# Kernel tuning notes

Hardware: AMD Instinct MI355X
Metric: run time of the kernel (lower is better)

Reference implementation:

```python
import jax, jax.numpy as jnp
import numpy as np

BIG = 1e10  # large finite value standing in for +inf in masked mins (grad-safe)


def setup_inputs() -> dict:
    key = jax.random.key(0)
    k1, k2, k3 = jax.random.split(key, 3)
    B, C, N = 16, 3, 4096
    x = jax.random.normal(k1, (B, C, N), dtype=jnp.float32)
    y = jax.random.normal(k2, (B, C, N), dtype=jnp.float32)
    mask = jax.random.randint(k3, (B, N), 0, 2, dtype=jnp.int32)
    return {"x": x, "y": y, "mask": mask}


def reference(x, y, mask):
    # x, y: (B, 3, N); mask: (B, N) with 1 = valid point
    xt = jnp.swapaxes(x, 1, 2)  # (B, N, 3)
    yt = jnp.swapaxes(y, 1, 2)  # (B, N, 3)
    xx = jnp.sum(xt * xt, axis=-1)  # (B, N)
    yy = jnp.sum(yt * yt, axis=-1)  # (B, N)
    # squared pairwise distances, P[b, n, m] = ||x_bn - y_bm||^2
    P = xx[:, :, None] + yy[:, None, :] - 2.0 * jnp.einsum("bnd,bmd->bnm", xt, yt)

    valid = mask.astype(bool)                 # (B, N)
    mf = mask.astype(P.dtype)                 # (B, N)
    cnt = jnp.sum(mf, axis=1)                 # (B,) number of valid points per batch

    # direction 1: for each y-point m, min over valid x-rows n; mean over valid m
    mins1 = jnp.min(jnp.where(valid[:, :, None], P, BIG), axis=1)  # (B, N)
    means1 = jnp.sum(mins1 * mf, axis=1) / cnt                      # (B,)

    # direction 2: for each x-point m, min over valid y-cols n; mean over valid m
    mins2 = jnp.min(jnp.where(valid[:, None, :], P, BIG), axis=2)  # (B, N)
    means2 = jnp.sum(mins2 * mf, axis=1) / cnt                      # (B,)

    return jnp.mean(means1) + jnp.mean(means2)
```

## Files before the change

### kernel.cpp

```cpp
#include <hip/hip_runtime.h>

typedef short bf16x8 __attribute__((ext_vector_type(8)));
typedef float f32x16 __attribute__((ext_vector_type(16)));

#define BIG_F 1e10f
constexpr int B = 16;
constexpr int N = 4096;
constexpr int COLS = 512;
constexpr int NCB = N / COLS;
constexpr int PASSES = 2;
constexpr int SUBROWS = 512;
constexpr int NSB = N / SUBROWS;

__device__ __forceinline__ void split(float v, unsigned& h, unsigned& l) {
    unsigned hb = __float_as_uint(v) & 0xFFFF0000u;
    h = hb >> 16;
    float r = v - __uint_as_float(hb);
    l = __float_as_uint(r) >> 16;
}

__device__ __forceinline__ float min3f(float a, float b, float c) {
    return fminf(fminf(a, b), c);
}

__device__ __forceinline__ float vmin16(f32x16 C) {
    float u0 = min3f(C[0], C[1], C[2]);
    float u1 = min3f(C[3], C[4], C[5]);
    float u2 = min3f(C[6], C[7], C[8]);
    float u3 = min3f(C[9], C[10], C[11]);
    float u4 = min3f(C[12], C[13], C[14]);
    return min3f(min3f(u0, u1, u2), fminf(u3, u4), C[15]);
}

__device__ __forceinline__ float4 min4(float4 a, float4 b) {
    return make_float4(fminf(a.x, b.x), fminf(a.y, b.y),
                       fminf(a.z, b.z), fminf(a.w, b.w));
}

#define DPP_MIN(v, ctrl)                                                      \
    v = fminf(v, __int_as_float(__builtin_amdgcn_update_dpp(                  \
            __float_as_int(v), __float_as_int(v), (ctrl), 0xF, 0xF, false)))

__global__ __launch_bounds__(256, 3) void chamfer_mfma(
    const float* __restrict__ x, const float* __restrict__ y,
    const int* __restrict__ mask,
    float* __restrict__ rowpart,
    float* __restrict__ colpart,
    float* __restrict__ out)
{
    const int blk = blockIdx.x;
    const int b   = blk >> 6;
    const int cb  = (blk >> 3) & 7;
    const int sub = blk & 7;
    const int t   = threadIdx.x;

    __shared__ __align__(16) unsigned short Bpack[2][COLS][8];
    __shared__ float colbuf[8][COLS];

    if (blk == 0 && t == 0) out[0] = 0.0f;

    const float* xb = x + (size_t)b * 3 * N;
    const float* yb = y + (size_t)b * 3 * N;
    const int*   mb = mask + b * N;

#pragma unroll
    for (int i = 0; i < 2; ++i) {
        int c = t + i * 256;
        int m = cb * COLS + c;
        float y0 = yb[m], y1 = yb[N + m], y2 = yb[2 * N + m];
        float madd = mb[m] ? 0.0f : BIG_F;
        float yy = fmaf(y2, y2, fmaf(y1, y1, y0 * y0)) + madd;
        unsigned h0, l0, h1, l1, h2, l2, qh, ql;
        split(y0, h0, l0);
        split(y1, h1, l1);
        split(y2, h2, l2);
        split(yy, qh, ql);
        unsigned u0 = h0 | (h1 << 16);
        unsigned u1 = h2 | (l0 << 16);
        unsigned u2 = l1 | (l2 << 16);
        uint4 w0 = { u0, u1, u2, u0 };
        uint4 w1 = { u1, u2, 0x3F803F80u, qh | (ql << 16) };
        *(uint4*)&Bpack[0][c][0] = w0;
        *(uint4*)&Bpack[1][c][0] = w1;
    }

    const int w    = t >> 6;
    const int L    = t & 63;
    const int half = L >> 5;
    const int lc   = L & 31;

    __syncthreads();

    const unsigned short* Bb = &Bpack[half][lc][0];
    float* cacc0 = &colbuf[w * 2 + half][lc];

    const f32x16 z16 = {0.f,0.f,0.f,0.f,0.f,0.f,0.f,0.f,
                        0.f,0.f,0.f,0.f,0.f,0.f,0.f,0.f};

    auto buildA = [&](int n) -> bf16x8 {
        float x0 = xb[n], x1 = xb[N + n], x2 = xb[2 * N + n];
        float madd = mb[n] ? 0.0f : BIG_F;
        float xx = fmaf(x2, x2, fmaf(x1, x1, x0 * x0)) + madd;
        unsigned h0, l0, h1, l1, h2, l2, xh, xl;
        split(-2.0f * x0, h0, l0);
        split(-2.0f * x1, h1, l1);
        split(-2.0f * x2, h2, l2);
        split(xx, xh, xl);
        uint4 wa;
        wa.x = half ? (l2 | (l0 << 16)) : (h0 | (h1 << 16));
        wa.y = half ? (l1 | (l2 << 16)) : (h2 | (h0 << 16));
        wa.z = half ? (xh | (xl << 16)) : (h1 | (h2 << 16));
        wa.w = half ? 0x3F803F80u       : (l0 | (l1 << 16));
        return *(bf16x8*)&wa;
    };

#pragma unroll 1
    for (int pass = 0; pass < PASSES; ++pass) {
        const int rowbase = sub * SUBROWS + pass * 256;
        bf16x8 afrA = buildA(rowbase + w * 32 + lc);
        bf16x8 afrB = buildA(rowbase + 128 + w * 32 + lc);

        float rmA[16], rmB[16];
#pragma unroll
        for (int r = 0; r < 16; ++r) { rmA[r] = 1e30f; rmB[r] = 1e30f; }

#pragma unroll 1
        for (int p = 0; p < 8; ++p) {
            bf16x8 bf0 = *(const bf16x8*)(Bb + p * 512);
            bf16x8 bf1 = *(const bf16x8*)(Bb + p * 512 + 256);
            f32x16 C0a = __builtin_amdgcn_mfma_f32_32x32x16_bf16(afrA, bf0, z16, 0, 0, 0);
            f32x16 C0b = __builtin_amdgcn_mfma_f32_32x32x16_bf16(afrB, bf0, z16, 0, 0, 0);
            f32x16 C1a = __builtin_amdgcn_mfma_f32_32x32x16_bf16(afrA, bf1, z16, 0, 0, 0);
            f32x16 C1b = __builtin_amdgcn_mfma_f32_32x32x16_bf16(afrB, bf1, z16, 0, 0, 0);
#pragma unroll
            for (int r = 0; r < 16; ++r) {
                rmA[r] = min3f(rmA[r], C0a[r], C1a[r]);
                rmB[r] = min3f(rmB[r], C0b[r], C1b[r]);
            }
            float v0 = fminf(vmin16(C0a), vmin16(C0b));
            float v1 = fminf(vmin16(C1a), vmin16(C1b));
            if (pass == 0) {
                cacc0[p * 64]      = v0;
                cacc0[p * 64 + 32] = v1;
            } else {
                cacc0[p * 64]      = fminf(cacc0[p * 64],      v0);
                cacc0[p * 64 + 32] = fminf(cacc0[p * 64 + 32], v1);
            }
        }

#pragma unroll
        for (int r = 0; r < 16; ++r) {
            DPP_MIN(rmA[r], 0xB1);   DPP_MIN(rmB[r], 0xB1);
            DPP_MIN(rmA[r], 0x4E);   DPP_MIN(rmB[r], 0x4E);
            DPP_MIN(rmA[r], 0x124);  DPP_MIN(rmB[r], 0x124);
            DPP_MIN(rmA[r], 0x128);  DPP_MIN(rmB[r], 0x128);
        }
        if ((lc & 15) == 0) {
            int sset = lc >> 4;
            float* rpA = rowpart + (((size_t)(b * NCB + cb)) * 2 + sset) * N
                       + rowbase + w * 32 + half * 4;
            float* rpB = rpA + 128;
            *(float4*)(rpA +  0) = make_float4(rmA[0],  rmA[1],  rmA[2],  rmA[3]);
            *(float4*)(rpA +  8) = make_float4(rmA[4],  rmA[5],  rmA[6],  rmA[7]);
            *(float4*)(rpA + 16) = make_float4(rmA[8],  rmA[9],  rmA[10], rmA[11]);
            *(float4*)(rpA + 24) = make_float4(rmA[12], rmA[13], rmA[14], rmA[15]);
            *(float4*)(rpB +  0) = make_float4(rmB[0],  rmB[1],  rmB[2],  rmB[3]);
            *(float4*)(rpB +  8) = make_float4(rmB[4],  rmB[5],  rmB[6],  rmB[7]);
            *(float4*)(rpB + 16) = make_float4(rmB[8],  rmB[9],  rmB[10], rmB[11]);
            *(float4*)(rpB + 24) = make_float4(rmB[12], rmB[13], rmB[14], rmB[15]);
        }
    }

    __syncthreads();
    if (t < 128) {
        const float4* cb4 = (const float4*)&colbuf[0][0];
        float4 v = cb4[t];
#pragma unroll
        for (int s = 1; s < 8; ++s) v = min4(v, cb4[s * 128 + t]);
        *(float4*)(colpart + ((size_t)b * NSB + sub) * N + cb * COLS + t * 4) = v;
    }
}

__global__ __launch_bounds__(256) void finalize_kernel(
    const int* __restrict__ mask,
    const float* __restrict__ rowpart, const float* __restrict__ colpart,
    float* __restrict__ out)
{
    const int b = blockIdx.x & 15;
    const int q = blockIdx.x >> 4;
    const int t = threadIdx.x;
    const int* mrow = mask + b * N;

    int cnt = 0;
    for (int i = t; i < N / 4; i += 256) {
        int4 mk = ((const int4*)mrow)[i];
        cnt += mk.x + mk.y + mk.z + mk.w;
    }

    const int p0 = q * 1024 + t * 4;
    const float* cp = colpart + (size_t)b * NSB * N + p0;
    const float* rp = rowpart + (size_t)b * NCB * 2 * N + p0;

    float4 mn = *(const float4*)cp;
    float4 rn = *(const float4*)rp;
#pragma unroll 8
    for (int pb = 1; pb < NCB * 2; ++pb) {
        rn = min4(rn, *(const float4*)(rp + (size_t)pb * N));
        if (pb < NSB)
            mn = min4(mn, *(const float4*)(cp + (size_t)pb * N));
    }
    int4 mk = *(const int4*)(mrow + p0);
    float s = (mk.x ? (mn.x + rn.x) : 0.f) + (mk.y ? (mn.y + rn.y) : 0.f)
            + (mk.z ? (mn.z + rn.z) : 0.f) + (mk.w ? (mn.w + rn.w) : 0.f);

    for (int off = 32; off > 0; off >>= 1) {
        s   += __shfl_down(s, off);
        cnt += __shfl_down(cnt, off);
    }
    __shared__ float rs[4];
    __shared__ int   rc[4];
    const int wv = t >> 6;
    if ((t & 63) == 0) { rs[wv] = s; rc[wv] = cnt; }
    __syncthreads();
    if (t == 0) {
        float S = rs[0] + rs[1] + rs[2] + rs[3];
        float C = (float)(rc[0] + rc[1] + rc[2] + rc[3]);
        atomicAdd(out, (S / C) * (1.0f / 16.0f));
    }
}

extern "C" void kernel_launch(void* const* d_in, const int* in_sizes, int n_in,
                              void* d_out, int out_size, void* d_ws, size_t ws_size,
                              hipStream_t stream) {
    const float* x    = (const float*)d_in[0];
    const float* y    = (const float*)d_in[1];
    const int*   mask = (const int*)d_in[2];

    float* rowpart = (float*)d_ws;
    float* colpart = rowpart + (size_t)B * NCB * 2 * N;

    chamfer_mfma<<<dim3(B * NCB * NSB), 256, 0, stream>>>(
        x, y, mask, rowpart, colpart, (float*)d_out);
    finalize_kernel<<<dim3(64), 256, 0, stream>>>(
        mask, rowpart, colpart, (float*)d_out);
}
```

Measured before the change: 85.49 us.

## Compute column minima via separate transposed-role blocks instead of in-tile reduction

Doubles the grid so each block handles one chamfer direction, swapping x and y roles so that both directions use the cheap row-min DPP reduction path. This removes the per-tile column-min reduction through vmin16 and the LDS colbuf buffer, plus its extra sync. In exchange the distance matrix is computed twice via MFMA, and the partial buffer layout is unified for the finalize kernel.

```diff
diff --git a/kernel.cpp b/kernel.cpp
--- a/kernel.cpp
+++ b/kernel.cpp
@@ -10,7 +10,8 @@
 constexpr int NCB = N / COLS;
 constexpr int PASSES = 2;
 constexpr int SUBROWS = 512;
-constexpr int NSB = N / SUBROWS;
+constexpr int NSUB = N / SUBROWS;
+constexpr size_t PARTSZ = (size_t)B * NCB * 2 * N;
 
 __device__ __forceinline__ void split(float v, unsigned& h, unsigned& l) {
     unsigned hb = __float_as_uint(v) & 0xFFFF0000u;
@@ -23,15 +24,6 @@
     return fminf(fminf(a, b), c);
 }
 
-__device__ __forceinline__ float vmin16(f32x16 C) {
-    float u0 = min3f(C[0], C[1], C[2]);
-    float u1 = min3f(C[3], C[4], C[5]);
-    float u2 = min3f(C[6], C[7], C[8]);
-    float u3 = min3f(C[9], C[10], C[11]);
-    float u4 = min3f(C[12], C[13], C[14]);
-    return min3f(min3f(u0, u1, u2), fminf(u3, u4), C[15]);
-}
-
 __device__ __forceinline__ float4 min4(float4 a, float4 b) {
     return make_float4(fminf(a.x, b.x), fminf(a.y, b.y),
                        fminf(a.z, b.z), fminf(a.w, b.w));
@@ -41,45 +33,63 @@
     v = fminf(v, __int_as_float(__builtin_amdgcn_update_dpp(                  \
             __float_as_int(v), __float_as_int(v), (ctrl), 0xF, 0xF, false)))
 
+__device__ __forceinline__ void rowstyle(float v0, float v1, float v2,
+                                         float madd, uint4& w0, uint4& w1) {
+    float s = fmaf(v2, v2, fmaf(v1, v1, v0 * v0)) + madd;
+    unsigned h0, l0, h1, l1, h2, l2, sh, sl;
+    split(-2.0f * v0, h0, l0);
+    split(-2.0f * v1, h1, l1);
+    split(-2.0f * v2, h2, l2);
+    split(s, sh, sl);
+    w0 = make_uint4(h0 | (h1 << 16), h2 | (h0 << 16), h1 | (h2 << 16), l0 | (l1 << 16));
+    w1 = make_uint4(l2 | (l0 << 16), l1 | (l2 << 16), sh | (sl << 16), 0x3F803F80u);
+}
+__device__ __forceinline__ void colstyle(float v0, float v1, float v2,
+                                         float madd, uint4& w0, uint4& w1) {
+    float s = fmaf(v2, v2, fmaf(v1, v1, v0 * v0)) + madd;
+    unsigned h0, l0, h1, l1, h2, l2, sh, sl;
+    split(v0, h0, l0);
+    split(v1, h1, l1);
+    split(v2, h2, l2);
+    split(s, sh, sl);
+    unsigned u0 = h0 | (h1 << 16), u1 = h2 | (l0 << 16), u2 = l1 | (l2 << 16);
+    w0 = make_uint4(u0, u1, u2, u0);
+    w1 = make_uint4(u1, u2, 0x3F803F80u, sh | (sl << 16));
+}
+
 __global__ __launch_bounds__(256, 3) void chamfer_mfma(
     const float* __restrict__ x, const float* __restrict__ y,
     const int* __restrict__ mask,
-    float* __restrict__ rowpart,
-    float* __restrict__ colpart,
+    float* __restrict__ part,
     float* __restrict__ out)
 {
-    const int blk = blockIdx.x;
-    const int b   = blk >> 6;
-    const int cb  = (blk >> 3) & 7;
-    const int sub = blk & 7;
-    const int t   = threadIdx.x;
+    const int blk  = blockIdx.x;
+    const int dir  = blk & 1;
+    const int rest = blk >> 1;
+    const int b    = rest >> 6;
+    const int cb   = (rest >> 3) & 7;
+    const int sub  = rest & 7;
+    const int t    = threadIdx.x;
 
     __shared__ __align__(16) unsigned short Bpack[2][COLS][8];
-    __shared__ float colbuf[8][COLS];
 
     if (blk == 0 && t == 0) out[0] = 0.0f;
 
-    const float* xb = x + (size_t)b * 3 * N;
-    const float* yb = y + (size_t)b * 3 * N;
-    const int*   mb = mask + b * N;
+    const float* rsrc = dir ? y : x;
+    const float* csrc = dir ? x : y;
+    const int*   mb   = mask + b * N;
+    const float* rb3  = rsrc + (size_t)b * 3 * N;
+    const float* cb3  = csrc + (size_t)b * 3 * N;
 
 #pragma unroll
     for (int i = 0; i < 2; ++i) {
         int c = t + i * 256;
         int m = cb * COLS + c;
-        float y0 = yb[m], y1 = yb[N + m], y2 = yb[2 * N + m];
+        float v0 = cb3[m], v1 = cb3[N + m], v2 = cb3[2 * N + m];
         float madd = mb[m] ? 0.0f : BIG_F;
-        float yy = fmaf(y2, y2, fmaf(y1, y1, y0 * y0)) + madd;
-        unsigned h0, l0, h1, l1, h2, l2, qh, ql;
-        split(y0, h0, l0);
-        split(y1, h1, l1);
-        split(y2, h2, l2);
-        split(yy, qh, ql);
-        unsigned u0 = h0 | (h1 << 16);
-        unsigned u1 = h2 | (l0 << 16);
-        unsigned u2 = l1 | (l2 << 16);
-        uint4 w0 = { u0, u1, u2, u0 };
-        uint4 w1 = { u1, u2, 0x3F803F80u, qh | (ql << 16) };
+        uint4 w0, w1;
+        if (dir) rowstyle(v0, v1, v2, madd, w0, w1);
+        else     colstyle(v0, v1, v2, madd, w0, w1);
         *(uint4*)&Bpack[0][c][0] = w0;
         *(uint4*)&Bpack[1][c][0] = w1;
     }
@@ -92,27 +102,21 @@
     __syncthreads();
 
     const unsigned short* Bb = &Bpack[half][lc][0];
-    float* cacc0 = &colbuf[w * 2 + half][lc];
 
     const f32x16 z16 = {0.f,0.f,0.f,0.f,0.f,0.f,0.f,0.f,
                         0.f,0.f,0.f,0.f,0.f,0.f,0.f,0.f};
 
     auto buildA = [&](int n) -> bf16x8 {
-        float x0 = xb[n], x1 = xb[N + n], x2 = xb[2 * N + n];
+        float v0 = rb3[n], v1 = rb3[N + n], v2 = rb3[2 * N + n];
         float madd = mb[n] ? 0.0f : BIG_F;
-        float xx = fmaf(x2, x2, fmaf(x1, x1, x0 * x0)) + madd;
-        unsigned h0, l0, h1, l1, h2, l2, xh, xl;
-        split(-2.0f * x0, h0, l0);
-        split(-2.0f * x1, h1, l1);
-        split(-2.0f * x2, h2, l2);
-        split(xx, xh, xl);
-        uint4 wa;
-        wa.x = half ? (l2 | (l0 << 16)) : (h0 | (h1 << 16));
-        wa.y = half ? (l1 | (l2 << 16)) : (h2 | (h0 << 16));
-        wa.z = half ? (xh | (xl << 16)) : (h1 | (h2 << 16));
-        wa.w = half ? 0x3F803F80u       : (l0 | (l1 << 16));
+        uint4 w0, w1;
+        if (dir) colstyle(v0, v1, v2, madd, w0, w1);
+        else     rowstyle(v0, v1, v2, madd, w0, w1);
+        uint4 wa = half ? w1 : w0;
         return *(bf16x8*)&wa;
     };
+
+    float* pbase = part + (size_t)dir * PARTSZ;
 
 #pragma unroll 1
     for (int pass = 0; pass < PASSES; ++pass) {
@@ -137,15 +141,6 @@
                 rmA[r] = min3f(rmA[r], C0a[r], C1a[r]);
                 rmB[r] = min3f(rmB[r], C0b[r], C1b[r]);
             }
-            float v0 = fminf(vmin16(C0a), vmin16(C0b));
-            float v1 = fminf(vmin16(C1a), vmin16(C1b));
-            if (pass == 0) {
-                cacc0[p * 64]      = v0;
-                cacc0[p * 64 + 32] = v1;
-            } else {
-                cacc0[p * 64]      = fminf(cacc0[p * 64],      v0);
-                cacc0[p * 64 + 32] = fminf(cacc0[p * 64 + 32], v1);
-            }
         }
 
 #pragma unroll
@@ -157,7 +152,7 @@
         }
         if ((lc & 15) == 0) {
             int sset = lc >> 4;
-            float* rpA = rowpart + (((size_t)(b * NCB + cb)) * 2 + sset) * N
+            float* rpA = pbase + (((size_t)(b * NCB + cb)) * 2 + sset) * N
                        + rowbase + w * 32 + half * 4;
             float* rpB = rpA + 128;
             *(float4*)(rpA +  0) = make_float4(rmA[0],  rmA[1],  rmA[2],  rmA[3]);
@@ -170,20 +165,11 @@
             *(float4*)(rpB + 24) = make_float4(rmB[12], rmB[13], rmB[14], rmB[15]);
         }
     }
-
-    __syncthreads();
-    if (t < 128) {
-        const float4* cb4 = (const float4*)&colbuf[0][0];
-        float4 v = cb4[t];
-#pragma unroll
-        for (int s = 1; s < 8; ++s) v = min4(v, cb4[s * 128 + t]);
-        *(float4*)(colpart + ((size_t)b * NSB + sub) * N + cb * COLS + t * 4) = v;
-    }
 }
 
 __global__ __launch_bounds__(256) void finalize_kernel(
     const int* __restrict__ mask,
-    const float* __restrict__ rowpart, const float* __restrict__ colpart,
+    const float* __restrict__ part,
     float* __restrict__ out)
 {
     const int b = blockIdx.x & 15;
@@ -198,16 +184,15 @@
     }
 
     const int p0 = q * 1024 + t * 4;
-    const float* cp = colpart + (size_t)b * NSB * N + p0;
-    const float* rp = rowpart + (size_t)b * NCB * 2 * N + p0;
-
-    float4 mn = *(const float4*)cp;
-    float4 rn = *(const float4*)rp;
+    const float* d0 = part + (size_t)b * NCB * 2 * N + p0;
+    const float* d1 = part + PARTSZ + (size_t)b * NCB * 2 * N + p0;
+
+    float4 rn = *(const float4*)d0;
+    float4 mn = *(const float4*)d1;
 #pragma unroll 8
     for (int pb = 1; pb < NCB * 2; ++pb) {
-        rn = min4(rn, *(const float4*)(rp + (size_t)pb * N));
-        if (pb < NSB)
-            mn = min4(mn, *(const float4*)(cp + (size_t)pb * N));
+        rn = min4(rn, *(const float4*)(d0 + (size_t)pb * N));
+        mn = min4(mn, *(const float4*)(d1 + (size_t)pb * N));
     }
     int4 mk = *(const int4*)(mrow + p0);
     float s = (mk.x ? (mn.x + rn.x) : 0.f) + (mk.y ? (mn.y + rn.y) : 0.f)
@@ -236,11 +221,10 @@
     const float* y    = (const float*)d_in[1];
     const int*   mask = (const int*)d_in[2];
 
-    float* rowpart = (float*)d_ws;
-    float* colpart = rowpart + (size_t)B * NCB * 2 * N;
-
-    chamfer_mfma<<<dim3(B * NCB * NSB), 256, 0, stream>>>(
-        x, y, mask, rowpart, colpart, (float*)d_out);
+    float* part = (float*)d_ws;
+
+    chamfer_mfma<<<dim3(2 * B * NCB * NSUB), 256, 0, stream>>>(
+        x, y, mask, part, (float*)d_out);
     finalize_kernel<<<dim3(64), 256, 0, stream>>>(
-        mask, rowpart, colpart, (float*)d_out);
-}
+        mask, part, (float*)d_out);
+}
```

New measurement: 92.42 us. +8.1%, slower.
